# Kernel tuning notes

Measured on AMD Instinct MI355X. Metric: run time of the kernel, lower is better.

## Reference

```python
import jax, jax.numpy as jnp
import numpy as np

N = 100          # num_objects
H = 128          # decoder_hidden
D = 128          # input_size (== H, required by the module's GRU linears)
REL = 7          # num_relative_features (use_3d=False)
E = N * (N - 1)  # fully-connected, no self loops
B = 32

_mask = ~np.eye(N, dtype=bool)
_SEND_NP, _RECV_NP = np.where(_mask)  # torch.where(~eye): rows=send, cols=recv
SEND = jnp.asarray(_SEND_NP, dtype=jnp.int32)
RECV = jnp.asarray(_RECV_NP, dtype=jnp.int32)


def setup_inputs() -> dict:
    key = jax.random.key(0)
    ks = jax.random.split(key, 34)
    def w(k, shape, scale=0.05):
        return jax.random.normal(k, shape, dtype=jnp.float32) * scale
    inp = {
        "inputs": jax.random.normal(ks[0], (B, N, D), jnp.float32),
        "edge_attr": jax.random.normal(ks[1], (B, E, REL + D), jnp.float32),
        "hidden": jax.random.normal(ks[2], (B, N, H), jnp.float32),
        # msg_mlp: Linear(2H,H) Tanh Linear(H,H) Tanh
        "msg_w1": w(ks[3], (2 * H, H)), "msg_b1": w(ks[4], (H,)),
        "msg_w2": w(ks[5], (H, H)),     "msg_b2": w(ks[6], (H,)),
        # present_msg_mlp: Linear(REL+D,H) ReLU Linear(H,H) ReLU
        "pm_w1": w(ks[7], (REL + D, H)), "pm_b1": w(ks[8], (H,)),
        "pm_w2": w(ks[9], (H, H)),       "pm_b2": w(ks[10], (H,)),
        # res_mlp: Linear(D,H) ReLU Linear(H,H) ReLU
        "res_w1": w(ks[11], (D, H)), "res_b1": w(ks[12], (H,)),
        "res_w2": w(ks[13], (H, H)), "res_b2": w(ks[14], (H,)),
        # GRU-style gates
        "ir_w": w(ks[15], (H, H)), "ir_b": w(ks[16], (H,)),
        "ii_w": w(ks[17], (H, H)), "ii_b": w(ks[18], (H,)),
        "in_w": w(ks[19], (H, H)), "in_b": w(ks[20], (H,)),
        "hr_w": w(ks[21], (H, H)),
        "hi_w": w(ks[22], (H, H)),
        "hh_w": w(ks[23], (H, H)),
        # out_mlp: Linear(H,H) ReLU Linear(H,H) ReLU Linear(H,D)
        "out_w1": w(ks[24], (H, H)), "out_b1": w(ks[25], (H,)),
        "out_w2": w(ks[26], (H, H)), "out_b2": w(ks[27], (H,)),
        "out_w3": w(ks[28], (H, D)), "out_b3": w(ks[29], (D,)),
    }
    return inp


def _scatter_mean(msgs, recv, num_nodes):
    # msgs: [B, E, H] -> [B, N, H], mean over incoming edges per node
    counts = jnp.zeros((num_nodes,), msgs.dtype).at[recv].add(1.0)
    summed = jnp.zeros((msgs.shape[0], num_nodes, msgs.shape[-1]), msgs.dtype)
    summed = summed.at[:, recv].add(msgs)
    return summed / counts[None, :, None]


def reference(inputs, edge_attr, hidden,
              msg_w1, msg_b1, msg_w2, msg_b2,
              pm_w1, pm_b1, pm_w2, pm_b2,
              res_w1, res_b1, res_w2, res_b2,
              ir_w, ir_b, ii_w, ii_b, in_w, in_b,
              hr_w, hi_w, hh_w,
              out_w1, out_b1, out_w2, out_b2, out_w3, out_b3):
    # gather hidden states along edges (dropout is identity: p=0 / eval)
    hm = jnp.concatenate([hidden[:, RECV], hidden[:, SEND]], axis=-1)  # [B,E,2H]
    hm = jnp.tanh(jnp.tanh(hm @ msg_w1 + msg_b1) @ msg_w2 + msg_b2)
    hidden_node = _scatter_mean(hm, RECV, N)                           # [B,N,H]

    pm = jax.nn.relu(jax.nn.relu(edge_attr @ pm_w1 + pm_b1) @ pm_w2 + pm_b2)
    present_node = _scatter_mean(pm, RECV, N)
    present_node = present_node + jax.nn.relu(
        jax.nn.relu(inputs @ res_w1 + res_b1) @ res_w2 + res_b2)

    r = jax.nn.sigmoid(present_node @ ir_w + ir_b + hidden_node @ hr_w)
    i = jax.nn.sigmoid(present_node @ ii_w + ii_b + hidden_node @ hi_w)
    n = jnp.tanh(present_node @ in_w + in_b + r * (hidden_node @ hh_w))
    hidden_new = (1.0 - i) * n + i * hidden

    pred = jax.nn.relu(hidden_new @ out_w1 + out_b1)
    pred = jax.nn.relu(pred @ out_w2 + out_b2)
    pred = pred @ out_w3 + out_b3
    return pred, hidden_new
```

## Files before the change

kernel.cpp:

```cpp
#include <hip/hip_runtime.h>

typedef unsigned short u16;
typedef unsigned int   u32;
typedef __attribute__((ext_vector_type(8))) short bf8;
typedef __attribute__((ext_vector_type(4))) float f4;

#define DF __device__ __forceinline__

DF float bf2f(u16 h){ u32 u = ((u32)h) << 16; float f; __builtin_memcpy(&f, &u, 4); return f; }
DF u16 f2bf(float f){ u32 u; __builtin_memcpy(&u, &f, 4); u = (u + 0x7FFFu + ((u >> 16) & 1u)) >> 16; return (u16)u; }
DF float fexp2(float x){ return __builtin_amdgcn_exp2f(x); }
DF float frcp (float x){ return __builtin_amdgcn_rcpf(x); }
DF float tanhF(float x){ float e = fexp2(2.8853900817779268f * x); return 1.0f - 2.0f * frcp(e + 1.0f); }
DF float sigF (float x){ return frcp(1.0f + fexp2(-1.4426950408889634f * x)); }
DF float4 ld4u(const float* p){ float4 v; __builtin_memcpy(&v, p, 16); return v; }
DF u32 cvtpk(float lo, float hi){ u32 r; asm("v_cvt_pk_bf16_f32 %0, %1, %2" : "=v"(r) : "v"(lo), "v"(hi)); return r; }

DF const bf8* fragp(const u16* packed, int w, int nt, int ks, int lane){
  return reinterpret_cast<const bf8*>(packed + (((w * 32 + nt * 4 + ks) * 64 + lane) * 8));
}
DF const bf8* fragp_pm1(const u16* packed, int nt, int ks, int lane){
  return reinterpret_cast<const bf8*>(packed + (((512 + nt * 5 + ks) * 64 + lane) * 8));
}

struct WPtrs { const float* p[16]; };

__global__ __launch_bounds__(256) void k_pack(WPtrs wp, u16* __restrict__ packed){
  int bi = blockIdx.x;
  int lane = threadIdx.x & 63, warp = threadIdx.x >> 6;
  if(bi == 16){
    const float* __restrict__ src = wp.p[14];
    u16* __restrict__ dst = packed + 512 * 64 * 8;
    for(int i = warp; i < 40; i += 4){
      int nt = i / 5, ks = i - nt * 5;
      int col = nt * 16 + (lane & 15);
      int kb  = ks * 32 + (lane >> 4) * 8;
      u16* o = dst + (i * 64 + lane) * 8;
      for(int j = 0; j < 8; j++){
        int row = kb + j;
        o[j] = (row < 135) ? f2bf(src[row * 128 + col]) : (u16)0;
      }
    }
    return;
  }
  const float* __restrict__ src = wp.p[bi];
  u16* __restrict__ dst = packed + bi * 32 * 64 * 8;
  for(int i = warp; i < 32; i += 4){
    int nt = i >> 2, ks = i & 3;
    int col = nt * 16 + (lane & 15);
    int kb  = ks * 32 + (lane >> 4) * 8;
    u16* o = dst + (i * 64 + lane) * 8;
    for(int j = 0; j < 8; j++) o[j] = f2bf(src[(kb + j) * 128 + col]);
  }
}

__global__ __launch_bounds__(512) void k_node_pre(
    const float* __restrict__ hidden, const float* __restrict__ inputs,
    const u16* __restrict__ packed,
    const float* __restrict__ res_b1, const float* __restrict__ res_b2,
    float* __restrict__ Ptop, float* __restrict__ Pbot, float* __restrict__ res2)
{
  __shared__ __align__(16) u16 hid[64 * 136];
  __shared__ __align__(16) u16 inp[64 * 136];
  __shared__ __align__(16) u16 t1s[64 * 136];
  int row0 = blockIdx.x * 64;
  int t = threadIdx.x, lane = t & 63, w = t >> 6;
  int lrow = lane & 15, lk = lane >> 4;
  for(int i = t; i < 64 * 128; i += 512){
    int rr = i >> 7, cc = i & 127;
    hid[rr * 136 + cc] = f2bf(hidden[(row0 + rr) * 128 + cc]);
    inp[rr * 136 + cc] = f2bf(inputs[(row0 + rr) * 128 + cc]);
  }
  int col = w * 16 + lrow;
  float rb1 = res_b1[col], rb2 = res_b2[col];
  __syncthreads();
  {
    bf8 f0[4], f1[4], f5[4];
    #pragma unroll
    for(int k = 0; k < 4; k++){
      f0[k] = *fragp(packed, 0, w, k, lane);
      f1[k] = *fragp(packed, 1, w, k, lane);
      f5[k] = *fragp(packed, 5, w, k, lane);
    }
    #pragma unroll
    for(int m = 0; m < 4; m++){
      bf8 a[4], a2[4];
      #pragma unroll
      for(int k = 0; k < 4; k++){
        a[k]  = *reinterpret_cast<const bf8*>(&hid[(m * 16 + lrow) * 136 + k * 32 + lk * 8]);
        a2[k] = *reinterpret_cast<const bf8*>(&inp[(m * 16 + lrow) * 136 + k * 32 + lk * 8]);
      }
      f4 c0 = {0.f,0.f,0.f,0.f}, c1 = {0.f,0.f,0.f,0.f}, c2 = {0.f,0.f,0.f,0.f};
      #pragma unroll
      for(int k = 0; k < 4; k++){
        c0 = __builtin_amdgcn_mfma_f32_16x16x32_bf16(a[k],  f0[k], c0, 0, 0, 0);
        c1 = __builtin_amdgcn_mfma_f32_16x16x32_bf16(a[k],  f1[k], c1, 0, 0, 0);
        c2 = __builtin_amdgcn_mfma_f32_16x16x32_bf16(a2[k], f5[k], c2, 0, 0, 0);
      }
      #pragma unroll
      for(int q = 0; q < 4; q++){
        int gr = row0 + m * 16 + lk * 4 + q;
        Ptop[gr * 128 + col] = c0[q];
        Pbot[gr * 128 + col] = c1[q];
        float v = c2[q] + rb1; v = v > 0.f ? v : 0.f;
        t1s[(m * 16 + lk * 4 + q) * 136 + col] = f2bf(v);
      }
    }
  }
  __syncthreads();
  {
    bf8 f6[4];
    #pragma unroll
    for(int k = 0; k < 4; k++) f6[k] = *fragp(packed, 6, w, k, lane);
    #pragma unroll
    for(int m = 0; m < 4; m++){
      bf8 a3[4];
      #pragma unroll
      for(int k = 0; k < 4; k++)
        a3[k] = *reinterpret_cast<const bf8*>(&t1s[(m * 16 + lrow) * 136 + k * 32 + lk * 8]);
      f4 c = {0.f,0.f,0.f,0.f};
      #pragma unroll
      for(int k = 0; k < 4; k++)
        c = __builtin_amdgcn_mfma_f32_16x16x32_bf16(a3[k], f6[k], c, 0, 0, 0);
      #pragma unroll
      for(int q = 0; q < 4; q++){
        float v = c[q] + rb2; v = v > 0.f ? v : 0.f;
        res2[(row0 + m * 16 + lk * 4 + q) * 128 + col] = v;
      }
    }
  }
}

__global__ __launch_bounds__(512, 4) void k_edge(
    const float* __restrict__ EA,
    const float* __restrict__ Ptop, const float* __restrict__ Pbot,
    const float* __restrict__ msg_b1, const float* __restrict__ msg_b2,
    const float* __restrict__ pm_b1, const float* __restrict__ pm_b2,
    const u16* __restrict__ packed,
    float* __restrict__ hnode, float* __restrict__ pnode)
{
  __shared__ __align__(16) u16 bufA[112 * 128];
  __shared__ __align__(16) u16 tail[112 * 8];
  char* bb = (char*)bufA;
  char* tb = (char*)tail;
  int blk = blockIdx.x;
  int b = blk / 100, r = blk - b * 100;
  int t = threadIdx.x, lane = t & 63, w = t >> 6;
  int lrow = lane & 15, lk = lane >> 4;

  {
    for(int i = t; i < 99 * 16; i += 512){
      int row = i >> 4, g = i & 15;
      int s = row + (row >= r ? 1 : 0);
      int e = s * 99 + (r < s ? r : r - 1);
      const float* rp = EA + ((size_t)(b * 9900 + e)) * 135 + g * 8;
      float4 v0 = ld4u(rp), v1 = ld4u(rp + 4);
      u32 pk[4] = {cvtpk(v0.x, v0.y), cvtpk(v0.z, v0.w), cvtpk(v1.x, v1.y), cvtpk(v1.z, v1.w)};
      *reinterpret_cast<uint4*>(bb + row * 256 + ((g ^ (row & 7)) << 4)) = *reinterpret_cast<const uint4*>(pk);
    }
    for(int row = t; row < 99; row += 512){
      int s = row + (row >= r ? 1 : 0);
      int e = s * 99 + (r < s ? r : r - 1);
      const float* rp = EA + ((size_t)(b * 9900 + e)) * 135 + 128;
      float4 v0 = ld4u(rp);
      u32 pk[4] = {cvtpk(v0.x, v0.y), cvtpk(v0.z, v0.w), cvtpk(rp[4], rp[5]), cvtpk(rp[6], 0.f)};
      *reinterpret_cast<uint4*>(tb + row * 16) = *reinterpret_cast<const uint4*>(pk);
    }
    bf8 w1[5];
    #pragma unroll
    for(int k = 0; k < 5; k++) w1[k] = *fragp_pm1(packed, w, k, lane);
    asm volatile("" : "+v"(w1[0]), "+v"(w1[1]), "+v"(w1[2]), "+v"(w1[3]), "+v"(w1[4]));
    float b1 = pm_b1[w * 16 + lrow];
    __syncthreads();

    f4 cA[4];
    #pragma unroll
    for(int m = 0; m < 4; m++){
      int arow = m * 16 + lrow, sw = arow & 7;
      bf8 a[4];
      #pragma unroll
      for(int k = 0; k < 4; k++)
        a[k] = *reinterpret_cast<const bf8*>(bb + arow * 256 + (((k * 4 + lk) ^ sw) << 4));
      bf8 a4 = {0,0,0,0,0,0,0,0};
      if(lk == 0) a4 = *reinterpret_cast<const bf8*>(tb + arow * 16);
      f4 c = {0.f,0.f,0.f,0.f};
      #pragma unroll
      for(int k = 0; k < 4; k++)
        c = __builtin_amdgcn_mfma_f32_16x16x32_bf16(a[k], w1[k], c, 0, 0, 0);
      c = __builtin_amdgcn_mfma_f32_16x16x32_bf16(a4, w1[4], c, 0, 0, 0);
      cA[m] = c;
    }
    __syncthreads();

    #pragma unroll
    for(int m = 0; m < 4; m++){
      #pragma unroll
      for(int qp = 0; qp < 2; qp++){
        float v0 = cA[m][2*qp]   + b1; v0 = v0 > 0.f ? v0 : 0.f;
        float u0 = cA[m][2*qp+1] + b1; u0 = u0 > 0.f ? u0 : 0.f;
        u32 p0 = cvtpk(v0, u0);
        int row0_ = m * 16 + lk * 4 + 2 * qp;
        int sw0 = (row0_ & 7) << 4, sw1 = ((row0_ + 1) & 7) << 4;
        *reinterpret_cast<u16*>(bb + row0_ * 256       + (((w * 16 + lrow) * 2) ^ sw0)) = (u16)p0;
        *reinterpret_cast<u16*>(bb + (row0_ + 1) * 256 + (((w * 16 + lrow) * 2) ^ sw1)) = (u16)(p0 >> 16);
      }
    }
    f4 cB[3];
    #pragma unroll
    for(int m = 0; m < 3; m++){
      int arow = (m + 4) * 16 + lrow, sw = arow & 7;
      bf8 a[4];
      #pragma unroll
      for(int k = 0; k < 4; k++)
        a[k] = *reinterpret_cast<const bf8*>(bb + arow * 256 + (((k * 4 + lk) ^ sw) << 4));
      bf8 a4 = {0,0,0,0,0,0,0,0};
      if(lk == 0) a4 = *reinterpret_cast<const bf8*>(tb + arow * 16);
      f4 c = {0.f,0.f,0.f,0.f};
      #pragma unroll
      for(int k = 0; k < 4; k++)
        c = __builtin_amdgcn_mfma_f32_16x16x32_bf16(a[k], w1[k], c, 0, 0, 0);
      c = __builtin_amdgcn_mfma_f32_16x16x32_bf16(a4, w1[4], c, 0, 0, 0);
      cB[m] = c;
    }
    __syncthreads();

    #pragma unroll
    for(int m = 0; m < 3; m++){
      #pragma unroll
      for(int qp = 0; qp < 2; qp++){
        float v0 = cB[m][2*qp]   + b1; v0 = v0 > 0.f ? v0 : 0.f;
        float u0 = cB[m][2*qp+1] + b1; u0 = u0 > 0.f ? u0 : 0.f;
        u32 p0 = cvtpk(v0, u0);
        int row0_ = (m + 4) * 16 + lk * 4 + 2 * qp;
        int sw0 = (row0_ & 7) << 4, sw1 = ((row0_ + 1) & 7) << 4;
        *reinterpret_cast<u16*>(bb + row0_ * 256       + (((w * 16 + lrow) * 2) ^ sw0)) = (u16)p0;
        *reinterpret_cast<u16*>(bb + (row0_ + 1) * 256 + (((w * 16 + lrow) * 2) ^ sw1)) = (u16)(p0 >> 16);
      }
    }
    __syncthreads();

    bf8 w2[4];
    #pragma unroll
    for(int k = 0; k < 4; k++) w2[k] = *fragp(packed, 15, w, k, lane);
    float b2 = pm_b2[w * 16 + lrow];
    float acc = 0.f;
    #pragma unroll
    for(int m = 0; m < 7; m++){
      int arow = m * 16 + lrow, sw = arow & 7;
      bf8 a[4];
      #pragma unroll
      for(int k = 0; k < 4; k++)
        a[k] = *reinterpret_cast<const bf8*>(bb + arow * 256 + (((k * 4 + lk) ^ sw) << 4));
      f4 c = {0.f,0.f,0.f,0.f};
      #pragma unroll
      for(int k = 0; k < 4; k++)
        c = __builtin_amdgcn_mfma_f32_16x16x32_bf16(a[k], w2[k], c, 0, 0, 0);
      #pragma unroll
      for(int q = 0; q < 4; q++){
        int rr = m * 16 + lk * 4 + q;
        if(rr < 99){ float v = c[q] + b2; acc += (v > 0.f ? v : 0.f); }
      }
    }
    acc += __shfl_xor(acc, 16); acc += __shfl_xor(acc, 32);
    if(lane < 16) pnode[((size_t)b * 100 + r) * 128 + w * 16 + lane] = acc * (1.0f / 99.0f);
  }
  __syncthreads();

  {
    bf8 w2[4];
    #pragma unroll
    for(int k = 0; k < 4; k++) w2[k] = *fragp(packed, 13, w, k, lane);
    float b2 = msg_b2[w * 16 + lrow];
    int c4 = t & 31;
    float4 pt = *reinterpret_cast<const float4*>(Ptop + ((size_t)b * 100 + r) * 128 + c4 * 4);
    float4 mb = *reinterpret_cast<const float4*>(msg_b1 + c4 * 4);
    pt.x += mb.x; pt.y += mb.y; pt.z += mb.z; pt.w += mb.w;
    for(int row = t >> 5; row < 99; row += 16){
      int s = row + (row >= r ? 1 : 0);
      float4 v = *reinterpret_cast<const float4*>(Pbot + ((size_t)b * 100 + s) * 128 + c4 * 4);
      u32 pk[2] = {cvtpk(tanhF(pt.x + v.x), tanhF(pt.y + v.y)),
                   cvtpk(tanhF(pt.z + v.z), tanhF(pt.w + v.w))};
      *reinterpret_cast<uint2*>(bb + row * 256 + ((8 * c4) ^ ((row & 7) << 4))) = *reinterpret_cast<const uint2*>(pk);
    }
    __syncthreads();
    float acc = 0.f;
    #pragma unroll
    for(int m = 0; m < 7; m++){
      int arow = m * 16 + lrow, sw = arow & 7;
      bf8 a[4];
      #pragma unroll
      for(int k = 0; k < 4; k++)
        a[k] = *reinterpret_cast<const bf8*>(bb + arow * 256 + (((k * 4 + lk) ^ sw) << 4));
      f4 c = {0.f,0.f,0.f,0.f};
      #pragma unroll
      for(int k = 0; k < 4; k++)
        c = __builtin_amdgcn_mfma_f32_16x16x32_bf16(a[k], w2[k], c, 0, 0, 0);
      #pragma unroll
      for(int q = 0; q < 4; q++){
        int rr = m * 16 + lk * 4 + q;
        if(rr < 99) acc += tanhF(c[q] + b2);
      }
    }
    acc += __shfl_xor(acc, 16); acc += __shfl_xor(acc, 32);
    if(lane < 16) hnode[((size_t)b * 100 + r) * 128 + w * 16 + lane] = acc * (1.0f / 99.0f);
  }
}

__global__ __launch_bounds__(512) void k_final(
    const float* __restrict__ hnode, const float* __restrict__ pnode,
    const float* __restrict__ res2, const float* __restrict__ hidden,
    const u16* __restrict__ packed,
    const float* __restrict__ ir_b, const float* __restrict__ ii_b, const float* __restrict__ in_b,
    const float* __restrict__ ob1, const float* __restrict__ ob2, const float* __restrict__ ob3,
    float* __restrict__ out_pred, float* __restrict__ out_hid)
{
  __shared__ __align__(16) u16 hn[64 * 136];
  __shared__ __align__(16) u16 pr[64 * 136];
  __shared__ __align__(16) u16 hw[64 * 136];
  int row0 = blockIdx.x * 64;
  int t = threadIdx.x, lane = t & 63, w = t >> 6;
  int lrow = lane & 15, lk = lane >> 4;
  for(int i = t; i < 64 * 128; i += 512){
    int rr = i >> 7, cc = i & 127;
    hn[rr * 136 + cc] = f2bf(hnode[(row0 + rr) * 128 + cc]);
    pr[rr * 136 + cc] = f2bf(pnode[(row0 + rr) * 128 + cc] + res2[(row0 + rr) * 128 + cc]);
  }
  int col = w * 16 + lrow;
  float bir = ir_b[col], bii = ii_b[col], bin = in_b[col];
  __syncthreads();
  #pragma unroll
  for(int m = 0; m < 4; m++){
    bf8 a[4], p[4];
    #pragma unroll
    for(int k = 0; k < 4; k++){
      a[k] = *reinterpret_cast<const bf8*>(&hn[(m * 16 + lrow) * 136 + k * 32 + lk * 8]);
      p[k] = *reinterpret_cast<const bf8*>(&pr[(m * 16 + lrow) * 136 + k * 32 + lk * 8]);
    }
    f4 cR = {0.f,0.f,0.f,0.f}, cI = {0.f,0.f,0.f,0.f}, cN = {0.f,0.f,0.f,0.f};
    f4 dR = {0.f,0.f,0.f,0.f}, dI = {0.f,0.f,0.f,0.f}, dN = {0.f,0.f,0.f,0.f};
    #pragma unroll
    for(int k = 0; k < 4; k++){
      cR = __builtin_amdgcn_mfma_f32_16x16x32_bf16(a[k], *fragp(packed, 2, w, k, lane), cR, 0, 0, 0);
      cI = __builtin_amdgcn_mfma_f32_16x16x32_bf16(a[k], *fragp(packed, 3, w, k, lane), cI, 0, 0, 0);
      cN = __builtin_amdgcn_mfma_f32_16x16x32_bf16(a[k], *fragp(packed, 4, w, k, lane), cN, 0, 0, 0);
      dR = __builtin_amdgcn_mfma_f32_16x16x32_bf16(p[k], *fragp(packed, 7, w, k, lane), dR, 0, 0, 0);
      dI = __builtin_amdgcn_mfma_f32_16x16x32_bf16(p[k], *fragp(packed, 8, w, k, lane), dI, 0, 0, 0);
      dN = __builtin_amdgcn_mfma_f32_16x16x32_bf16(p[k], *fragp(packed, 9, w, k, lane), dN, 0, 0, 0);
    }
    #pragma unroll
    for(int q = 0; q < 4; q++){
      int gr = row0 + m * 16 + lk * 4 + q;
      float rv = sigF(dR[q] + bir + cR[q]);
      float iv = sigF(dI[q] + bii + cI[q]);
      float nv = tanhF(dN[q] + bin + rv * cN[q]);
      float hold = hidden[gr * 128 + col];
      float hnew = (1.f - iv) * nv + iv * hold;
      out_hid[gr * 128 + col] = hnew;
      hw[(m * 16 + lk * 4 + q) * 136 + col] = f2bf(hnew);
    }
  }
  __syncthreads();
  {
    bf8 m10[4];
    #pragma unroll
    for(int k = 0; k < 4; k++) m10[k] = *fragp(packed, 10, w, k, lane);
    float bb = ob1[col];
    #pragma unroll
    for(int m = 0; m < 4; m++){
      f4 c = {0.f,0.f,0.f,0.f};
      #pragma unroll
      for(int k = 0; k < 4; k++){
        bf8 a = *reinterpret_cast<const bf8*>(&hw[(m * 16 + lrow) * 136 + k * 32 + lk * 8]);
        c = __builtin_amdgcn_mfma_f32_16x16x32_bf16(a, m10[k], c, 0, 0, 0);
      }
      #pragma unroll
      for(int q = 0; q < 4; q++){
        float v = c[q] + bb; v = v > 0.f ? v : 0.f;
        hn[(m * 16 + lk * 4 + q) * 136 + col] = f2bf(v);
      }
    }
  }
  __syncthreads();
  {
    bf8 m11[4];
    #pragma unroll
    for(int k = 0; k < 4; k++) m11[k] = *fragp(packed, 11, w, k, lane);
    float bb = ob2[col];
    #pragma unroll
    for(int m = 0; m < 4; m++){
      f4 c = {0.f,0.f,0.f,0.f};
      #pragma unroll
      for(int k = 0; k < 4; k++){
        bf8 a = *reinterpret_cast<const bf8*>(&hn[(m * 16 + lrow) * 136 + k * 32 + lk * 8]);
        c = __builtin_amdgcn_mfma_f32_16x16x32_bf16(a, m11[k], c, 0, 0, 0);
      }
      #pragma unroll
      for(int q = 0; q < 4; q++){
        float v = c[q] + bb; v = v > 0.f ? v : 0.f;
        pr[(m * 16 + lk * 4 + q) * 136 + col] = f2bf(v);
      }
    }
  }
  __syncthreads();
  {
    bf8 m12[4];
    #pragma unroll
    for(int k = 0; k < 4; k++) m12[k] = *fragp(packed, 12, w, k, lane);
    float bb = ob3[col];
    #pragma unroll
    for(int m = 0; m < 4; m++){
      f4 c = {0.f,0.f,0.f,0.f};
      #pragma unroll
      for(int k = 0; k < 4; k++){
        bf8 a = *reinterpret_cast<const bf8*>(&pr[(m * 16 + lrow) * 136 + k * 32 + lk * 8]);
        c = __builtin_amdgcn_mfma_f32_16x16x32_bf16(a, m12[k], c, 0, 0, 0);
      }
      #pragma unroll
      for(int q = 0; q < 4; q++)
        out_pred[(row0 + m * 16 + lk * 4 + q) * 128 + col] = c[q] + bb;
    }
  }
}

extern "C" void kernel_launch(void* const* d_in, const int* in_sizes, int n_in,
                              void* d_out, int out_size, void* d_ws, size_t ws_size,
                              hipStream_t stream)
{
  const float* inputs = (const float*)d_in[0];
  const float* edge   = (const float*)d_in[1];
  const float* hidden = (const float*)d_in[2];
  const float* msg_w1 = (const float*)d_in[3];
  const float* msg_b1 = (const float*)d_in[4];
  const float* msg_w2 = (const float*)d_in[5];
  const float* msg_b2 = (const float*)d_in[6];
  const float* pm_w1  = (const float*)d_in[7];
  const float* pm_b1  = (const float*)d_in[8];
  const float* pm_w2  = (const float*)d_in[9];
  const float* pm_b2  = (const float*)d_in[10];
  const float* res_w1 = (const float*)d_in[11];
  const float* res_b1 = (const float*)d_in[12];
  const float* res_w2 = (const float*)d_in[13];
  const float* res_b2 = (const float*)d_in[14];
  const float* ir_w = (const float*)d_in[15]; const float* ir_b = (const float*)d_in[16];
  const float* ii_w = (const float*)d_in[17]; const float* ii_b = (const float*)d_in[18];
  const float* in_w = (const float*)d_in[19]; const float* in_b = (const float*)d_in[20];
  const float* hr_w = (const float*)d_in[21];
  const float* hi_w = (const float*)d_in[22];
  const float* hh_w = (const float*)d_in[23];
  const float* out_w1 = (const float*)d_in[24]; const float* out_b1 = (const float*)d_in[25];
  const float* out_w2 = (const float*)d_in[26]; const float* out_b2 = (const float*)d_in[27];
  const float* out_w3 = (const float*)d_in[28]; const float* out_b3 = (const float*)d_in[29];

  char* ws = (char*)d_ws;
  u16*   packed = (u16*)ws;
  float* Ptop   = (float*)(ws + (1 << 20));
  float* Pbot   = (float*)(ws + (1 << 20) + 1 * 1638400);
  float* res2   = (float*)(ws + (1 << 20) + 2 * 1638400);
  float* hnode  = (float*)(ws + (1 << 20) + 3 * 1638400);
  float* pnode  = (float*)(ws + (1 << 20) + 4 * 1638400);

  WPtrs wp;
  wp.p[0]  = msg_w1;
  wp.p[1]  = msg_w1 + 128 * 128;
  wp.p[2]  = hr_w;  wp.p[3]  = hi_w;  wp.p[4]  = hh_w;
  wp.p[5]  = res_w1; wp.p[6] = res_w2;
  wp.p[7]  = ir_w;  wp.p[8]  = ii_w;  wp.p[9]  = in_w;
  wp.p[10] = out_w1; wp.p[11] = out_w2; wp.p[12] = out_w3;
  wp.p[13] = msg_w2; wp.p[14] = pm_w1; wp.p[15] = pm_w2;

  k_pack<<<17, 256, 0, stream>>>(wp, packed);
  k_node_pre<<<50, 512, 0, stream>>>(hidden, inputs, packed, res_b1, res_b2, Ptop, Pbot, res2);
  k_edge<<<3200, 512, 0, stream>>>(edge, Ptop, Pbot, msg_b1, msg_b2, pm_b1, pm_b2,
                                   packed, hnode, pnode);
  float* outp = (float*)d_out;
  k_final<<<50, 512, 0, stream>>>(hnode, pnode, res2, hidden, packed,
                                  ir_b, ii_b, in_b, out_b1, out_b2, out_b3,
                                  outp, outp + 32 * 100 * 128);
}
```

Before: 129.6 us.

## Split each receiver's edges across two blocks and combine partial sums later

The edge kernel now runs two blocks per (batch, receiver) pair, covering 64 and 35 incoming edges. Each block writes unnormalised partial sums into separate halves of the workspace, and k_final adds the two halves and divides by 99. This doubles the grid and shrinks shared memory per block, which should raise occupancy and parallelism, and it removes the second pass over 3 row groups. In exchange the second block wastes MFMA work on padded rows, and the extra partial buffers cost more global traffic. k_final also hoists its gate weight fragments into registers before the loop.

```diff
diff --git a/kernel.cpp b/kernel.cpp
--- a/kernel.cpp
+++ b/kernel.cpp
@@ -137,160 +137,110 @@
     const float* __restrict__ msg_b1, const float* __restrict__ msg_b2,
     const float* __restrict__ pm_b1, const float* __restrict__ pm_b2,
     const u16* __restrict__ packed,
-    float* __restrict__ hnode, float* __restrict__ pnode)
+    float* __restrict__ hnode_h, float* __restrict__ pnode_h)
 {
-  __shared__ __align__(16) u16 bufA[112 * 128];
-  __shared__ __align__(16) u16 tail[112 * 8];
-  char* bb = (char*)bufA;
+  __shared__ __align__(16) u16 ea [64 * 128];
+  __shared__ __align__(16) u16 h1b[64 * 128];
+  __shared__ __align__(16) u16 tail[64 * 8];
+  char* eb = (char*)ea;
+  char* hb = (char*)h1b;
   char* tb = (char*)tail;
-  int blk = blockIdx.x;
+  int bid = blockIdx.x;
+  int hh = bid & 1;
+  int blk = bid >> 1;
   int b = blk / 100, r = blk - b * 100;
+  int gbase = hh << 6;
+  int vlim = hh ? 35 : 64;
   int t = threadIdx.x, lane = t & 63, w = t >> 6;
   int lrow = lane & 15, lk = lane >> 4;
-
-  {
-    for(int i = t; i < 99 * 16; i += 512){
-      int row = i >> 4, g = i & 15;
-      int s = row + (row >= r ? 1 : 0);
+  float* __restrict__ pnode = pnode_h + (size_t)hh * 3200 * 128;
+  float* __restrict__ hnode = hnode_h + (size_t)hh * 3200 * 128;
+
+  for(int i = t; i < 64 * 16; i += 512){
+    int local = i >> 4, g = i & 15;
+    int gr = gbase + local;
+    if(gr < 99){
+      int s = gr + (gr >= r ? 1 : 0);
       int e = s * 99 + (r < s ? r : r - 1);
       const float* rp = EA + ((size_t)(b * 9900 + e)) * 135 + g * 8;
       float4 v0 = ld4u(rp), v1 = ld4u(rp + 4);
       u32 pk[4] = {cvtpk(v0.x, v0.y), cvtpk(v0.z, v0.w), cvtpk(v1.x, v1.y), cvtpk(v1.z, v1.w)};
-      *reinterpret_cast<uint4*>(bb + row * 256 + ((g ^ (row & 7)) << 4)) = *reinterpret_cast<const uint4*>(pk);
-    }
-    for(int row = t; row < 99; row += 512){
-      int s = row + (row >= r ? 1 : 0);
+      *reinterpret_cast<uint4*>(eb + local * 256 + ((g ^ (local & 7)) << 4)) = *reinterpret_cast<const uint4*>(pk);
+    }
+  }
+  if(t < 64){
+    int gr = gbase + t;
+    if(gr < 99){
+      int s = gr + (gr >= r ? 1 : 0);
       int e = s * 99 + (r < s ? r : r - 1);
       const float* rp = EA + ((size_t)(b * 9900 + e)) * 135 + 128;
       float4 v0 = ld4u(rp);
       u32 pk[4] = {cvtpk(v0.x, v0.y), cvtpk(v0.z, v0.w), cvtpk(rp[4], rp[5]), cvtpk(rp[6], 0.f)};
-      *reinterpret_cast<uint4*>(tb + row * 16) = *reinterpret_cast<const uint4*>(pk);
-    }
-    bf8 w1[5];
-    #pragma unroll
-    for(int k = 0; k < 5; k++) w1[k] = *fragp_pm1(packed, w, k, lane);
-    asm volatile("" : "+v"(w1[0]), "+v"(w1[1]), "+v"(w1[2]), "+v"(w1[3]), "+v"(w1[4]));
-    float b1 = pm_b1[w * 16 + lrow];
-    __syncthreads();
-
-    f4 cA[4];
-    #pragma unroll
-    for(int m = 0; m < 4; m++){
-      int arow = m * 16 + lrow, sw = arow & 7;
-      bf8 a[4];
-      #pragma unroll
-      for(int k = 0; k < 4; k++)
-        a[k] = *reinterpret_cast<const bf8*>(bb + arow * 256 + (((k * 4 + lk) ^ sw) << 4));
-      bf8 a4 = {0,0,0,0,0,0,0,0};
-      if(lk == 0) a4 = *reinterpret_cast<const bf8*>(tb + arow * 16);
-      f4 c = {0.f,0.f,0.f,0.f};
-      #pragma unroll
-      for(int k = 0; k < 4; k++)
-        c = __builtin_amdgcn_mfma_f32_16x16x32_bf16(a[k], w1[k], c, 0, 0, 0);
-      c = __builtin_amdgcn_mfma_f32_16x16x32_bf16(a4, w1[4], c, 0, 0, 0);
-      cA[m] = c;
-    }
-    __syncthreads();
-
-    #pragma unroll
-    for(int m = 0; m < 4; m++){
-      #pragma unroll
-      for(int qp = 0; qp < 2; qp++){
-        float v0 = cA[m][2*qp]   + b1; v0 = v0 > 0.f ? v0 : 0.f;
-        float u0 = cA[m][2*qp+1] + b1; u0 = u0 > 0.f ? u0 : 0.f;
-        u32 p0 = cvtpk(v0, u0);
-        int row0_ = m * 16 + lk * 4 + 2 * qp;
-        int sw0 = (row0_ & 7) << 4, sw1 = ((row0_ + 1) & 7) << 4;
-        *reinterpret_cast<u16*>(bb + row0_ * 256       + (((w * 16 + lrow) * 2) ^ sw0)) = (u16)p0;
-        *reinterpret_cast<u16*>(bb + (row0_ + 1) * 256 + (((w * 16 + lrow) * 2) ^ sw1)) = (u16)(p0 >> 16);
-      }
-    }
-    f4 cB[3];
-    #pragma unroll
-    for(int m = 0; m < 3; m++){
-      int arow = (m + 4) * 16 + lrow, sw = arow & 7;
-      bf8 a[4];
-      #pragma unroll
-      for(int k = 0; k < 4; k++)
-        a[k] = *reinterpret_cast<const bf8*>(bb + arow * 256 + (((k * 4 + lk) ^ sw) << 4));
-      bf8 a4 = {0,0,0,0,0,0,0,0};
-      if(lk == 0) a4 = *reinterpret_cast<const bf8*>(tb + arow * 16);
-      f4 c = {0.f,0.f,0.f,0.f};
-      #pragma unroll
-      for(int k = 0; k < 4; k++)
-        c = __builtin_amdgcn_mfma_f32_16x16x32_bf16(a[k], w1[k], c, 0, 0, 0);
-      c = __builtin_amdgcn_mfma_f32_16x16x32_bf16(a4, w1[4], c, 0, 0, 0);
-      cB[m] = c;
-    }
-    __syncthreads();
-
-    #pragma unroll
-    for(int m = 0; m < 3; m++){
-      #pragma unroll
-      for(int qp = 0; qp < 2; qp++){
-        float v0 = cB[m][2*qp]   + b1; v0 = v0 > 0.f ? v0 : 0.f;
-        float u0 = cB[m][2*qp+1] + b1; u0 = u0 > 0.f ? u0 : 0.f;
-        u32 p0 = cvtpk(v0, u0);
-        int row0_ = (m + 4) * 16 + lk * 4 + 2 * qp;
-        int sw0 = (row0_ & 7) << 4, sw1 = ((row0_ + 1) & 7) << 4;
-        *reinterpret_cast<u16*>(bb + row0_ * 256       + (((w * 16 + lrow) * 2) ^ sw0)) = (u16)p0;
-        *reinterpret_cast<u16*>(bb + (row0_ + 1) * 256 + (((w * 16 + lrow) * 2) ^ sw1)) = (u16)(p0 >> 16);
-      }
-    }
-    __syncthreads();
-
-    bf8 w2[4];
-    #pragma unroll
-    for(int k = 0; k < 4; k++) w2[k] = *fragp(packed, 15, w, k, lane);
-    float b2 = pm_b2[w * 16 + lrow];
-    float acc = 0.f;
-    #pragma unroll
-    for(int m = 0; m < 7; m++){
-      int arow = m * 16 + lrow, sw = arow & 7;
-      bf8 a[4];
-      #pragma unroll
-      for(int k = 0; k < 4; k++)
-        a[k] = *reinterpret_cast<const bf8*>(bb + arow * 256 + (((k * 4 + lk) ^ sw) << 4));
-      f4 c = {0.f,0.f,0.f,0.f};
-      #pragma unroll
-      for(int k = 0; k < 4; k++)
-        c = __builtin_amdgcn_mfma_f32_16x16x32_bf16(a[k], w2[k], c, 0, 0, 0);
-      #pragma unroll
-      for(int q = 0; q < 4; q++){
-        int rr = m * 16 + lk * 4 + q;
-        if(rr < 99){ float v = c[q] + b2; acc += (v > 0.f ? v : 0.f); }
-      }
-    }
-    acc += __shfl_xor(acc, 16); acc += __shfl_xor(acc, 32);
-    if(lane < 16) pnode[((size_t)b * 100 + r) * 128 + w * 16 + lane] = acc * (1.0f / 99.0f);
-  }
-  __syncthreads();
-
-  {
-    bf8 w2[4];
-    #pragma unroll
-    for(int k = 0; k < 4; k++) w2[k] = *fragp(packed, 13, w, k, lane);
-    float b2 = msg_b2[w * 16 + lrow];
+      *reinterpret_cast<uint4*>(tb + t * 16) = *reinterpret_cast<const uint4*>(pk);
+    }
+  }
+  bf8 w1[5];
+  #pragma unroll
+  for(int k = 0; k < 5; k++) w1[k] = *fragp_pm1(packed, w, k, lane);
+  asm volatile("" : "+v"(w1[0]), "+v"(w1[1]), "+v"(w1[2]), "+v"(w1[3]), "+v"(w1[4]));
+  float b1 = pm_b1[w * 16 + lrow];
+  __syncthreads();
+
+  #pragma unroll
+  for(int m = 0; m < 4; m++){
+    int arow = m * 16 + lrow, sw = arow & 7;
+    bf8 a[4];
+    #pragma unroll
+    for(int k = 0; k < 4; k++)
+      a[k] = *reinterpret_cast<const bf8*>(eb + arow * 256 + (((k * 4 + lk) ^ sw) << 4));
+    bf8 a4 = {0,0,0,0,0,0,0,0};
+    if(lk == 0) a4 = *reinterpret_cast<const bf8*>(tb + arow * 16);
+    f4 c = {0.f,0.f,0.f,0.f};
+    #pragma unroll
+    for(int k = 0; k < 4; k++)
+      c = __builtin_amdgcn_mfma_f32_16x16x32_bf16(a[k], w1[k], c, 0, 0, 0);
+    c = __builtin_amdgcn_mfma_f32_16x16x32_bf16(a4, w1[4], c, 0, 0, 0);
+    #pragma unroll
+    for(int qp = 0; qp < 2; qp++){
+      float v0 = c[2*qp]   + b1; v0 = v0 > 0.f ? v0 : 0.f;
+      float u0 = c[2*qp+1] + b1; u0 = u0 > 0.f ? u0 : 0.f;
+      u32 p = cvtpk(v0, u0);
+      int row0_ = m * 16 + lk * 4 + 2 * qp;
+      int sw0 = (row0_ & 7) << 4, sw1 = ((row0_ + 1) & 7) << 4;
+      *reinterpret_cast<u16*>(hb + row0_ * 256       + (((w * 16 + lrow) * 2) ^ sw0)) = (u16)p;
+      *reinterpret_cast<u16*>(hb + (row0_ + 1) * 256 + (((w * 16 + lrow) * 2) ^ sw1)) = (u16)(p >> 16);
+    }
+  }
+  __syncthreads();
+
+  {
     int c4 = t & 31;
     float4 pt = *reinterpret_cast<const float4*>(Ptop + ((size_t)b * 100 + r) * 128 + c4 * 4);
     float4 mb = *reinterpret_cast<const float4*>(msg_b1 + c4 * 4);
     pt.x += mb.x; pt.y += mb.y; pt.z += mb.z; pt.w += mb.w;
-    for(int row = t >> 5; row < 99; row += 16){
-      int s = row + (row >= r ? 1 : 0);
+    for(int local = t >> 5; local < vlim; local += 16){
+      int gr = gbase + local;
+      int s = gr + (gr >= r ? 1 : 0);
       float4 v = *reinterpret_cast<const float4*>(Pbot + ((size_t)b * 100 + s) * 128 + c4 * 4);
       u32 pk[2] = {cvtpk(tanhF(pt.x + v.x), tanhF(pt.y + v.y)),
                    cvtpk(tanhF(pt.z + v.z), tanhF(pt.w + v.w))};
-      *reinterpret_cast<uint2*>(bb + row * 256 + ((8 * c4) ^ ((row & 7) << 4))) = *reinterpret_cast<const uint2*>(pk);
-    }
-    __syncthreads();
+      *reinterpret_cast<uint2*>(eb + local * 256 + ((8 * c4) ^ ((local & 7) << 4))) = *reinterpret_cast<const uint2*>(pk);
+    }
+  }
+  {
+    bf8 w2[4];
+    #pragma unroll
+    for(int k = 0; k < 4; k++) w2[k] = *fragp(packed, 15, w, k, lane);
+    asm volatile("" : "+v"(w2[0]), "+v"(w2[1]), "+v"(w2[2]), "+v"(w2[3]));
+    float b2 = pm_b2[w * 16 + lrow];
     float acc = 0.f;
     #pragma unroll
-    for(int m = 0; m < 7; m++){
+    for(int m = 0; m < 4; m++){
       int arow = m * 16 + lrow, sw = arow & 7;
       bf8 a[4];
       #pragma unroll
       for(int k = 0; k < 4; k++)
-        a[k] = *reinterpret_cast<const bf8*>(bb + arow * 256 + (((k * 4 + lk) ^ sw) << 4));
+        a[k] = *reinterpret_cast<const bf8*>(hb + arow * 256 + (((k * 4 + lk) ^ sw) << 4));
       f4 c = {0.f,0.f,0.f,0.f};
       #pragma unroll
       for(int k = 0; k < 4; k++)
@@ -298,16 +248,45 @@
       #pragma unroll
       for(int q = 0; q < 4; q++){
         int rr = m * 16 + lk * 4 + q;
-        if(rr < 99) acc += tanhF(c[q] + b2);
+        if(rr < vlim){ float v = c[q] + b2; acc += (v > 0.f ? v : 0.f); }
       }
     }
     acc += __shfl_xor(acc, 16); acc += __shfl_xor(acc, 32);
-    if(lane < 16) hnode[((size_t)b * 100 + r) * 128 + w * 16 + lane] = acc * (1.0f / 99.0f);
+    if(lane < 16) pnode[((size_t)b * 100 + r) * 128 + w * 16 + lane] = acc;
+  }
+  __syncthreads();
+
+  {
+    bf8 w2[4];
+    #pragma unroll
+    for(int k = 0; k < 4; k++) w2[k] = *fragp(packed, 13, w, k, lane);
+    asm volatile("" : "+v"(w2[0]), "+v"(w2[1]), "+v"(w2[2]), "+v"(w2[3]));
+    float b2 = msg_b2[w * 16 + lrow];
+    float acc = 0.f;
+    #pragma unroll
+    for(int m = 0; m < 4; m++){
+      int arow = m * 16 + lrow, sw = arow & 7;
+      bf8 a[4];
+      #pragma unroll
+      for(int k = 0; k < 4; k++)
+        a[k] = *reinterpret_cast<const bf8*>(eb + arow * 256 + (((k * 4 + lk) ^ sw) << 4));
+      f4 c = {0.f,0.f,0.f,0.f};
+      #pragma unroll
+      for(int k = 0; k < 4; k++)
+        c = __builtin_amdgcn_mfma_f32_16x16x32_bf16(a[k], w2[k], c, 0, 0, 0);
+      #pragma unroll
+      for(int q = 0; q < 4; q++){
+        int rr = m * 16 + lk * 4 + q;
+        if(rr < vlim) acc += tanhF(c[q] + b2);
+      }
+    }
+    acc += __shfl_xor(acc, 16); acc += __shfl_xor(acc, 32);
+    if(lane < 16) hnode[((size_t)b * 100 + r) * 128 + w * 16 + lane] = acc;
   }
 }
 
 __global__ __launch_bounds__(512) void k_final(
-    const float* __restrict__ hnode, const float* __restrict__ pnode,
+    const float* __restrict__ hnode_h, const float* __restrict__ pnode_h,
     const float* __restrict__ res2, const float* __restrict__ hidden,
     const u16* __restrict__ packed,
     const float* __restrict__ ir_b, const float* __restrict__ ii_b, const float* __restrict__ in_b,
@@ -317,15 +296,29 @@
   __shared__ __align__(16) u16 hn[64 * 136];
   __shared__ __align__(16) u16 pr[64 * 136];
   __shared__ __align__(16) u16 hw[64 * 136];
+  const float inv99 = 1.0f / 99.0f;
   int row0 = blockIdx.x * 64;
   int t = threadIdx.x, lane = t & 63, w = t >> 6;
   int lrow = lane & 15, lk = lane >> 4;
+  const float* hA = hnode_h;              const float* hB = hnode_h + (size_t)3200 * 128;
+  const float* pA = pnode_h;              const float* pB = pnode_h + (size_t)3200 * 128;
   for(int i = t; i < 64 * 128; i += 512){
     int rr = i >> 7, cc = i & 127;
-    hn[rr * 136 + cc] = f2bf(hnode[(row0 + rr) * 128 + cc]);
-    pr[rr * 136 + cc] = f2bf(pnode[(row0 + rr) * 128 + cc] + res2[(row0 + rr) * 128 + cc]);
+    size_t gi = (size_t)(row0 + rr) * 128 + cc;
+    hn[rr * 136 + cc] = f2bf((hA[gi] + hB[gi]) * inv99);
+    pr[rr * 136 + cc] = f2bf((pA[gi] + pB[gi]) * inv99 + res2[gi]);
   }
   int col = w * 16 + lrow;
+  bf8 mhr[4], mhi[4], mhh[4], mir[4], mii[4], min_[4];
+  #pragma unroll
+  for(int k = 0; k < 4; k++){
+    mhr[k]  = *fragp(packed, 2, w, k, lane);
+    mhi[k]  = *fragp(packed, 3, w, k, lane);
+    mhh[k]  = *fragp(packed, 4, w, k, lane);
+    mir[k]  = *fragp(packed, 7, w, k, lane);
+    mii[k]  = *fragp(packed, 8, w, k, lane);
+    min_[k] = *fragp(packed, 9, w, k, lane);
+  }
   float bir = ir_b[col], bii = ii_b[col], bin = in_b[col];
   __syncthreads();
   #pragma unroll
@@ -340,12 +333,12 @@
     f4 dR = {0.f,0.f,0.f,0.f}, dI = {0.f,0.f,0.f,0.f}, dN = {0.f,0.f,0.f,0.f};
     #pragma unroll
     for(int k = 0; k < 4; k++){
-      cR = __builtin_amdgcn_mfma_f32_16x16x32_bf16(a[k], *fragp(packed, 2, w, k, lane), cR, 0, 0, 0);
-      cI = __builtin_amdgcn_mfma_f32_16x16x32_bf16(a[k], *fragp(packed, 3, w, k, lane), cI, 0, 0, 0);
-      cN = __builtin_amdgcn_mfma_f32_16x16x32_bf16(a[k], *fragp(packed, 4, w, k, lane), cN, 0, 0, 0);
-      dR = __builtin_amdgcn_mfma_f32_16x16x32_bf16(p[k], *fragp(packed, 7, w, k, lane), dR, 0, 0, 0);
-      dI = __builtin_amdgcn_mfma_f32_16x16x32_bf16(p[k], *fragp(packed, 8, w, k, lane), dI, 0, 0, 0);
-      dN = __builtin_amdgcn_mfma_f32_16x16x32_bf16(p[k], *fragp(packed, 9, w, k, lane), dN, 0, 0, 0);
+      cR = __builtin_amdgcn_mfma_f32_16x16x32_bf16(a[k], mhr[k],  cR, 0, 0, 0);
+      cI = __builtin_amdgcn_mfma_f32_16x16x32_bf16(a[k], mhi[k],  cI, 0, 0, 0);
+      cN = __builtin_amdgcn_mfma_f32_16x16x32_bf16(a[k], mhh[k],  cN, 0, 0, 0);
+      dR = __builtin_amdgcn_mfma_f32_16x16x32_bf16(p[k], mir[k],  dR, 0, 0, 0);
+      dI = __builtin_amdgcn_mfma_f32_16x16x32_bf16(p[k], mii[k],  dI, 0, 0, 0);
+      dN = __builtin_amdgcn_mfma_f32_16x16x32_bf16(p[k], min_[k], dN, 0, 0, 0);
     }
     #pragma unroll
     for(int q = 0; q < 4; q++){
@@ -452,12 +445,13 @@
   const float* out_w3 = (const float*)d_in[28]; const float* out_b3 = (const float*)d_in[29];
 
   char* ws = (char*)d_ws;
-  u16*   packed = (u16*)ws;
-  float* Ptop   = (float*)(ws + (1 << 20));
-  float* Pbot   = (float*)(ws + (1 << 20) + 1 * 1638400);
-  float* res2   = (float*)(ws + (1 << 20) + 2 * 1638400);
-  float* hnode  = (float*)(ws + (1 << 20) + 3 * 1638400);
-  float* pnode  = (float*)(ws + (1 << 20) + 4 * 1638400);
+  const size_t NODE = 3200 * 128 * 4;
+  u16*   packed  = (u16*)ws;
+  float* Ptop    = (float*)(ws + (1 << 20));
+  float* Pbot    = (float*)(ws + (1 << 20) + 1 * NODE);
+  float* res2    = (float*)(ws + (1 << 20) + 2 * NODE);
+  float* hnode_h = (float*)(ws + (1 << 20) + 3 * NODE);
+  float* pnode_h = (float*)(ws + (1 << 20) + 5 * NODE);
 
   WPtrs wp;
   wp.p[0]  = msg_w1;
@@ -470,10 +464,10 @@
 
   k_pack<<<17, 256, 0, stream>>>(wp, packed);
   k_node_pre<<<50, 512, 0, stream>>>(hidden, inputs, packed, res_b1, res_b2, Ptop, Pbot, res2);
-  k_edge<<<3200, 512, 0, stream>>>(edge, Ptop, Pbot, msg_b1, msg_b2, pm_b1, pm_b2,
-                                   packed, hnode, pnode);
+  k_edge<<<6400, 512, 0, stream>>>(edge, Ptop, Pbot, msg_b1, msg_b2, pm_b1, pm_b2,
+                                   packed, hnode_h, pnode_h);
   float* outp = (float*)d_out;
-  k_final<<<50, 512, 0, stream>>>(hnode, pnode, res2, hidden, packed,
+  k_final<<<50, 512, 0, stream>>>(hnode_h, pnode_h, res2, hidden, packed,
                                   ir_b, ii_b, in_b, out_b1, out_b2, out_b3,
                                   outp, outp + 32 * 100 * 128);
 }
```

Result: no change. 131.2 us (+1.3%).

## Make edge kernel persistent with weights hoisted into registers across blocks

Applied to the files above, without the earlier changes.

The edge kernel changes from 3200 one-shot blocks to 512 persistent blocks, each looping over (batch, receiver) pairs. The pm_w1, pm_w2 and msg_w2 fragments and their biases are loaded once into registers before the loop instead of once per block. Launch bounds drop from 4 to 2 blocks per CU to leave room for the extra live registers. The final kernel also preloads its six gate weight fragment sets before the main loop. The cost is lower occupancy and less latency hiding for the edge-attribute gathers, and 3200 work items over 512 blocks leaves the load slightly uneven.

```diff
diff --git a/kernel.cpp b/kernel.cpp
--- a/kernel.cpp
+++ b/kernel.cpp
@@ -131,7 +131,7 @@
   }
 }
 
-__global__ __launch_bounds__(512, 4) void k_edge(
+__global__ __launch_bounds__(512, 2) void k_edge(
     const float* __restrict__ EA,
     const float* __restrict__ Ptop, const float* __restrict__ Pbot,
     const float* __restrict__ msg_b1, const float* __restrict__ msg_b2,
@@ -143,12 +143,25 @@
   __shared__ __align__(16) u16 tail[112 * 8];
   char* bb = (char*)bufA;
   char* tb = (char*)tail;
-  int blk = blockIdx.x;
-  int b = blk / 100, r = blk - b * 100;
   int t = threadIdx.x, lane = t & 63, w = t >> 6;
   int lrow = lane & 15, lk = lane >> 4;
 
-  {
+  bf8 w1[5], w2p[4], w2m[4];
+  #pragma unroll
+  for(int k = 0; k < 5; k++) w1[k] = *fragp_pm1(packed, w, k, lane);
+  #pragma unroll
+  for(int k = 0; k < 4; k++){ w2p[k] = *fragp(packed, 15, w, k, lane); w2m[k] = *fragp(packed, 13, w, k, lane); }
+  asm volatile("" : "+v"(w1[0]), "+v"(w1[1]), "+v"(w1[2]), "+v"(w1[3]), "+v"(w1[4]));
+  asm volatile("" : "+v"(w2p[0]), "+v"(w2p[1]), "+v"(w2p[2]), "+v"(w2p[3]));
+  asm volatile("" : "+v"(w2m[0]), "+v"(w2m[1]), "+v"(w2m[2]), "+v"(w2m[3]));
+  float b1 = pm_b1[w * 16 + lrow];
+  float b2p = pm_b2[w * 16 + lrow];
+  float b2m = msg_b2[w * 16 + lrow];
+  const float inv99 = 1.0f / 99.0f;
+
+  for(int blk = blockIdx.x; blk < 3200; blk += 512){
+    int b = blk / 100, r = blk - b * 100;
+
     for(int i = t; i < 99 * 16; i += 512){
       int row = i >> 4, g = i & 15;
       int s = row + (row >= r ? 1 : 0);
@@ -166,11 +179,6 @@
       u32 pk[4] = {cvtpk(v0.x, v0.y), cvtpk(v0.z, v0.w), cvtpk(rp[4], rp[5]), cvtpk(rp[6], 0.f)};
       *reinterpret_cast<uint4*>(tb + row * 16) = *reinterpret_cast<const uint4*>(pk);
     }
-    bf8 w1[5];
-    #pragma unroll
-    for(int k = 0; k < 5; k++) w1[k] = *fragp_pm1(packed, w, k, lane);
-    asm volatile("" : "+v"(w1[0]), "+v"(w1[1]), "+v"(w1[2]), "+v"(w1[3]), "+v"(w1[4]));
-    float b1 = pm_b1[w * 16 + lrow];
     __syncthreads();
 
     f4 cA[4];
@@ -198,11 +206,11 @@
       for(int qp = 0; qp < 2; qp++){
         float v0 = cA[m][2*qp]   + b1; v0 = v0 > 0.f ? v0 : 0.f;
         float u0 = cA[m][2*qp+1] + b1; u0 = u0 > 0.f ? u0 : 0.f;
-        u32 p0 = cvtpk(v0, u0);
+        u32 p = cvtpk(v0, u0);
         int row0_ = m * 16 + lk * 4 + 2 * qp;
         int sw0 = (row0_ & 7) << 4, sw1 = ((row0_ + 1) & 7) << 4;
-        *reinterpret_cast<u16*>(bb + row0_ * 256       + (((w * 16 + lrow) * 2) ^ sw0)) = (u16)p0;
-        *reinterpret_cast<u16*>(bb + (row0_ + 1) * 256 + (((w * 16 + lrow) * 2) ^ sw1)) = (u16)(p0 >> 16);
+        *reinterpret_cast<u16*>(bb + row0_ * 256       + (((w * 16 + lrow) * 2) ^ sw0)) = (u16)p;
+        *reinterpret_cast<u16*>(bb + (row0_ + 1) * 256 + (((w * 16 + lrow) * 2) ^ sw1)) = (u16)(p >> 16);
       }
     }
     f4 cB[3];
@@ -230,79 +238,77 @@
       for(int qp = 0; qp < 2; qp++){
         float v0 = cB[m][2*qp]   + b1; v0 = v0 > 0.f ? v0 : 0.f;
         float u0 = cB[m][2*qp+1] + b1; u0 = u0 > 0.f ? u0 : 0.f;
-        u32 p0 = cvtpk(v0, u0);
+        u32 p = cvtpk(v0, u0);
         int row0_ = (m + 4) * 16 + lk * 4 + 2 * qp;
         int sw0 = (row0_ & 7) << 4, sw1 = ((row0_ + 1) & 7) << 4;
-        *reinterpret_cast<u16*>(bb + row0_ * 256       + (((w * 16 + lrow) * 2) ^ sw0)) = (u16)p0;
-        *reinterpret_cast<u16*>(bb + (row0_ + 1) * 256 + (((w * 16 + lrow) * 2) ^ sw1)) = (u16)(p0 >> 16);
-      }
-    }
-    __syncthreads();
-
-    bf8 w2[4];
-    #pragma unroll
-    for(int k = 0; k < 4; k++) w2[k] = *fragp(packed, 15, w, k, lane);
-    float b2 = pm_b2[w * 16 + lrow];
-    float acc = 0.f;
-    #pragma unroll
-    for(int m = 0; m < 7; m++){
-      int arow = m * 16 + lrow, sw = arow & 7;
-      bf8 a[4];
-      #pragma unroll
-      for(int k = 0; k < 4; k++)
-        a[k] = *reinterpret_cast<const bf8*>(bb + arow * 256 + (((k * 4 + lk) ^ sw) << 4));
-      f4 c = {0.f,0.f,0.f,0.f};
-      #pragma unroll
-      for(int k = 0; k < 4; k++)
-        c = __builtin_amdgcn_mfma_f32_16x16x32_bf16(a[k], w2[k], c, 0, 0, 0);
-      #pragma unroll
-      for(int q = 0; q < 4; q++){
-        int rr = m * 16 + lk * 4 + q;
-        if(rr < 99){ float v = c[q] + b2; acc += (v > 0.f ? v : 0.f); }
-      }
-    }
-    acc += __shfl_xor(acc, 16); acc += __shfl_xor(acc, 32);
-    if(lane < 16) pnode[((size_t)b * 100 + r) * 128 + w * 16 + lane] = acc * (1.0f / 99.0f);
-  }
-  __syncthreads();
-
-  {
-    bf8 w2[4];
-    #pragma unroll
-    for(int k = 0; k < 4; k++) w2[k] = *fragp(packed, 13, w, k, lane);
-    float b2 = msg_b2[w * 16 + lrow];
-    int c4 = t & 31;
-    float4 pt = *reinterpret_cast<const float4*>(Ptop + ((size_t)b * 100 + r) * 128 + c4 * 4);
-    float4 mb = *reinterpret_cast<const float4*>(msg_b1 + c4 * 4);
-    pt.x += mb.x; pt.y += mb.y; pt.z += mb.z; pt.w += mb.w;
-    for(int row = t >> 5; row < 99; row += 16){
-      int s = row + (row >= r ? 1 : 0);
-      float4 v = *reinterpret_cast<const float4*>(Pbot + ((size_t)b * 100 + s) * 128 + c4 * 4);
-      u32 pk[2] = {cvtpk(tanhF(pt.x + v.x), tanhF(pt.y + v.y)),
-                   cvtpk(tanhF(pt.z + v.z), tanhF(pt.w + v.w))};
-      *reinterpret_cast<uint2*>(bb + row * 256 + ((8 * c4) ^ ((row & 7) << 4))) = *reinterpret_cast<const uint2*>(pk);
-    }
-    __syncthreads();
-    float acc = 0.f;
-    #pragma unroll
-    for(int m = 0; m < 7; m++){
-      int arow = m * 16 + lrow, sw = arow & 7;
-      bf8 a[4];
-      #pragma unroll
-      for(int k = 0; k < 4; k++)
-        a[k] = *reinterpret_cast<const bf8*>(bb + arow * 256 + (((k * 4 + lk) ^ sw) << 4));
-      f4 c = {0.f,0.f,0.f,0.f};
-      #pragma unroll
-      for(int k = 0; k < 4; k++)
-        c = __builtin_amdgcn_mfma_f32_16x16x32_bf16(a[k], w2[k], c, 0, 0, 0);
-      #pragma unroll
-      for(int q = 0; q < 4; q++){
-        int rr = m * 16 + lk * 4 + q;
-        if(rr < 99) acc += tanhF(c[q] + b2);
-      }
-    }
-    acc += __shfl_xor(acc, 16); acc += __shfl_xor(acc, 32);
-    if(lane < 16) hnode[((size_t)b * 100 + r) * 128 + w * 16 + lane] = acc * (1.0f / 99.0f);
+        *reinterpret_cast<u16*>(bb + row0_ * 256       + (((w * 16 + lrow) * 2) ^ sw0)) = (u16)p;
+        *reinterpret_cast<u16*>(bb + (row0_ + 1) * 256 + (((w * 16 + lrow) * 2) ^ sw1)) = (u16)(p >> 16);
+      }
+    }
+    __syncthreads();
+
+    {
+      float acc = 0.f;
+      #pragma unroll
+      for(int m = 0; m < 7; m++){
+        int arow = m * 16 + lrow, sw = arow & 7;
+        bf8 a[4];
+        #pragma unroll
+        for(int k = 0; k < 4; k++)
+          a[k] = *reinterpret_cast<const bf8*>(bb + arow * 256 + (((k * 4 + lk) ^ sw) << 4));
+        f4 c = {0.f,0.f,0.f,0.f};
+        #pragma unroll
+        for(int k = 0; k < 4; k++)
+          c = __builtin_amdgcn_mfma_f32_16x16x32_bf16(a[k], w2p[k], c, 0, 0, 0);
+        #pragma unroll
+        for(int q = 0; q < 4; q++){
+          int rr = m * 16 + lk * 4 + q;
+          if(rr < 99){ float v = c[q] + b2p; acc += (v > 0.f ? v : 0.f); }
+        }
+      }
+      acc += __shfl_xor(acc, 16); acc += __shfl_xor(acc, 32);
+      if(lane < 16) pnode[((size_t)b * 100 + r) * 128 + w * 16 + lane] = acc * inv99;
+    }
+    __syncthreads();
+
+    {
+      int c4 = t & 31;
+      float4 pt = *reinterpret_cast<const float4*>(Ptop + ((size_t)b * 100 + r) * 128 + c4 * 4);
+      float4 mb = *reinterpret_cast<const float4*>(msg_b1 + c4 * 4);
+      pt.x += mb.x; pt.y += mb.y; pt.z += mb.z; pt.w += mb.w;
+      for(int row = t >> 5; row < 99; row += 16){
+        int s = row + (row >= r ? 1 : 0);
+        float4 v = *reinterpret_cast<const float4*>(Pbot + ((size_t)b * 100 + s) * 128 + c4 * 4);
+        u32 pk[2] = {cvtpk(tanhF(pt.x + v.x), tanhF(pt.y + v.y)),
+                     cvtpk(tanhF(pt.z + v.z), tanhF(pt.w + v.w))};
+        *reinterpret_cast<uint2*>(bb + row * 256 + ((8 * c4) ^ ((row & 7) << 4))) = *reinterpret_cast<const uint2*>(pk);
+      }
+    }
+    __syncthreads();
+
+    {
+      float acc = 0.f;
+      #pragma unroll
+      for(int m = 0; m < 7; m++){
+        int arow = m * 16 + lrow, sw = arow & 7;
+        bf8 a[4];
+        #pragma unroll
+        for(int k = 0; k < 4; k++)
+          a[k] = *reinterpret_cast<const bf8*>(bb + arow * 256 + (((k * 4 + lk) ^ sw) << 4));
+        f4 c = {0.f,0.f,0.f,0.f};
+        #pragma unroll
+        for(int k = 0; k < 4; k++)
+          c = __builtin_amdgcn_mfma_f32_16x16x32_bf16(a[k], w2m[k], c, 0, 0, 0);
+        #pragma unroll
+        for(int q = 0; q < 4; q++){
+          int rr = m * 16 + lk * 4 + q;
+          if(rr < 99) acc += tanhF(c[q] + b2m);
+        }
+      }
+      acc += __shfl_xor(acc, 16); acc += __shfl_xor(acc, 32);
+      if(lane < 16) hnode[((size_t)b * 100 + r) * 128 + w * 16 + lane] = acc * inv99;
+    }
+    __syncthreads();
   }
 }
 
@@ -322,10 +328,21 @@
   int lrow = lane & 15, lk = lane >> 4;
   for(int i = t; i < 64 * 128; i += 512){
     int rr = i >> 7, cc = i & 127;
-    hn[rr * 136 + cc] = f2bf(hnode[(row0 + rr) * 128 + cc]);
-    pr[rr * 136 + cc] = f2bf(pnode[(row0 + rr) * 128 + cc] + res2[(row0 + rr) * 128 + cc]);
+    size_t gi = (size_t)(row0 + rr) * 128 + cc;
+    hn[rr * 136 + cc] = f2bf(hnode[gi]);
+    pr[rr * 136 + cc] = f2bf(pnode[gi] + res2[gi]);
   }
   int col = w * 16 + lrow;
+  bf8 mhr[4], mhi[4], mhh[4], mir[4], mii[4], min_[4];
+  #pragma unroll
+  for(int k = 0; k < 4; k++){
+    mhr[k]  = *fragp(packed, 2, w, k, lane);
+    mhi[k]  = *fragp(packed, 3, w, k, lane);
+    mhh[k]  = *fragp(packed, 4, w, k, lane);
+    mir[k]  = *fragp(packed, 7, w, k, lane);
+    mii[k]  = *fragp(packed, 8, w, k, lane);
+    min_[k] = *fragp(packed, 9, w, k, lane);
+  }
   float bir = ir_b[col], bii = ii_b[col], bin = in_b[col];
   __syncthreads();
   #pragma unroll
@@ -340,12 +357,12 @@
     f4 dR = {0.f,0.f,0.f,0.f}, dI = {0.f,0.f,0.f,0.f}, dN = {0.f,0.f,0.f,0.f};
     #pragma unroll
     for(int k = 0; k < 4; k++){
-      cR = __builtin_amdgcn_mfma_f32_16x16x32_bf16(a[k], *fragp(packed, 2, w, k, lane), cR, 0, 0, 0);
-      cI = __builtin_amdgcn_mfma_f32_16x16x32_bf16(a[k], *fragp(packed, 3, w, k, lane), cI, 0, 0, 0);
-      cN = __builtin_amdgcn_mfma_f32_16x16x32_bf16(a[k], *fragp(packed, 4, w, k, lane), cN, 0, 0, 0);
-      dR = __builtin_amdgcn_mfma_f32_16x16x32_bf16(p[k], *fragp(packed, 7, w, k, lane), dR, 0, 0, 0);
-      dI = __builtin_amdgcn_mfma_f32_16x16x32_bf16(p[k], *fragp(packed, 8, w, k, lane), dI, 0, 0, 0);
-      dN = __builtin_amdgcn_mfma_f32_16x16x32_bf16(p[k], *fragp(packed, 9, w, k, lane), dN, 0, 0, 0);
+      cR = __builtin_amdgcn_mfma_f32_16x16x32_bf16(a[k], mhr[k],  cR, 0, 0, 0);
+      cI = __builtin_amdgcn_mfma_f32_16x16x32_bf16(a[k], mhi[k],  cI, 0, 0, 0);
+      cN = __builtin_amdgcn_mfma_f32_16x16x32_bf16(a[k], mhh[k],  cN, 0, 0, 0);
+      dR = __builtin_amdgcn_mfma_f32_16x16x32_bf16(p[k], mir[k],  dR, 0, 0, 0);
+      dI = __builtin_amdgcn_mfma_f32_16x16x32_bf16(p[k], mii[k],  dI, 0, 0, 0);
+      dN = __builtin_amdgcn_mfma_f32_16x16x32_bf16(p[k], min_[k], dN, 0, 0, 0);
     }
     #pragma unroll
     for(int q = 0; q < 4; q++){
@@ -452,12 +469,13 @@
   const float* out_w3 = (const float*)d_in[28]; const float* out_b3 = (const float*)d_in[29];
 
   char* ws = (char*)d_ws;
+  const size_t NODE = 3200 * 128 * 4;
   u16*   packed = (u16*)ws;
   float* Ptop   = (float*)(ws + (1 << 20));
-  float* Pbot   = (float*)(ws + (1 << 20) + 1 * 1638400);
-  float* res2   = (float*)(ws + (1 << 20) + 2 * 1638400);
-  float* hnode  = (float*)(ws + (1 << 20) + 3 * 1638400);
-  float* pnode  = (float*)(ws + (1 << 20) + 4 * 1638400);
+  float* Pbot   = (float*)(ws + (1 << 20) + 1 * NODE);
+  float* res2   = (float*)(ws + (1 << 20) + 2 * NODE);
+  float* hnode  = (float*)(ws + (1 << 20) + 3 * NODE);
+  float* pnode  = (float*)(ws + (1 << 20) + 4 * NODE);
 
   WPtrs wp;
   wp.p[0]  = msg_w1;
@@ -470,8 +488,8 @@
 
   k_pack<<<17, 256, 0, stream>>>(wp, packed);
   k_node_pre<<<50, 512, 0, stream>>>(hidden, inputs, packed, res_b1, res_b2, Ptop, Pbot, res2);
-  k_edge<<<3200, 512, 0, stream>>>(edge, Ptop, Pbot, msg_b1, msg_b2, pm_b1, pm_b2,
-                                   packed, hnode, pnode);
+  k_edge<<<512, 512, 0, stream>>>(edge, Ptop, Pbot, msg_b1, msg_b2, pm_b1, pm_b2,
+                                  packed, hnode, pnode);
   float* outp = (float*)d_out;
   k_final<<<50, 512, 0, stream>>>(hnode, pnode, res2, hidden, packed,
                                   ir_b, ii_b, in_b, out_b1, out_b2, out_b3,
```

Result: slower. 163.2 us (+25.9%).
